# Optimization experiments

Measured on AMD Instinct MI355X. Metric: run time of the kernel, lower is better.

Reference implementation:

```python
import jax, jax.numpy as jnp
import numpy as np
import math

B, S, E, H = 4, 1024, 768, 12
HD = E // H

def setup_inputs() -> dict:
    key = jax.random.key(0)
    ks = jax.random.split(key, 13)
    inp = {
        'query': jax.random.normal(ks[0], (B, S, E), jnp.float32),
        'key':   jax.random.normal(ks[1], (B, S, E), jnp.float32),
        'value': jax.random.normal(ks[2], (B, S, E), jnp.float32),
        'mask':  jax.random.randint(ks[3], (B, S, S), 0, 2, jnp.int32),
    }
    scale = 1.0 / math.sqrt(E)
    for i, nm in enumerate(['q', 'k', 'v', 'o']):
        inp[f'W{nm}'] = jax.random.normal(ks[4 + 2 * i], (E, E), jnp.float32) * scale
        inp[f'b{nm}'] = jax.random.normal(ks[5 + 2 * i], (E,), jnp.float32) * 0.01
    return inp


def reference(query, key, value, mask, Wq, bq, Wk, bk, Wv, bv, Wo, bo):
    # QKV projections (torch Linear: x @ W.T + b), split into heads -> [B,H,S,HD]
    def proj(x, W, b):
        y = x @ W.T + b
        return y.reshape(B, S, H, HD).transpose(0, 2, 1, 3)

    q = proj(query, Wq, bq)
    k = proj(key, Wk, bk)
    v = proj(value, Wv, bv)

    scores = jnp.einsum('bhqd,bhkd->bhqk', q, k) / jnp.sqrt(jnp.float32(HD))
    m = mask[:, None, :, :]  # [B,1,S,S] broadcast over heads
    # multiply-then-masked_fill semantics of the original module
    scores = scores * m.astype(scores.dtype)
    scores = jnp.where(m == 0, -jnp.inf, scores)
    attn = jax.nn.softmax(scores, axis=-1)
    # nan_to_num for fully-masked rows (all -inf -> NaN -> 0)
    attn = jnp.where(jnp.isnan(attn), 0.0, attn)
    # dropout omitted (eval/deterministic reference)
    xv = jnp.einsum('bhqk,bhkd->bhqd', attn, v)
    xv = xv.transpose(0, 2, 1, 3).reshape(B, S, E)
    out = xv @ Wo.T + bo
    return out
```

## Files before the change

kernel.cpp:

```cpp
#include <hip/hip_runtime.h>

typedef __bf16 bf16x8 __attribute__((ext_vector_type(8)));
typedef float floatx4 __attribute__((ext_vector_type(4)));

#define B_ 4
#define S_ 1024
#define E_ 768
#define H_ 12
#define HD_ 64

__device__ __forceinline__ void async16(const void* g, void* l) {
  __builtin_amdgcn_global_load_lds((const __attribute__((address_space(1))) void*)g,
                                   (__attribute__((address_space(3))) void*)l, 16, 0, 0);
}

__device__ __forceinline__ floatx4 mfma16(bf16x8 a, bf16x8 b, floatx4 c) {
  return __builtin_amdgcn_mfma_f32_16x16x32_bf16(a, b, c, 0, 0, 0);
}

__device__ __forceinline__ bf16x8 cvt8(float4 a, float4 b) {
  bf16x8 o;
  o[0] = (__bf16)a.x; o[1] = (__bf16)a.y; o[2] = (__bf16)a.z; o[3] = (__bf16)a.w;
  o[4] = (__bf16)b.x; o[5] = (__bf16)b.y; o[6] = (__bf16)b.z; o[7] = (__bf16)b.w;
  return o;
}

__global__ __launch_bounds__(256) void prep_kernel(
    const float* __restrict__ w0, const float* __restrict__ w1,
    const float* __restrict__ w2, const float* __restrict__ w3,
    const int* __restrict__ mask,
    __bf16* __restrict__ wb, unsigned long long* __restrict__ bm) {
  const int bx = blockIdx.x;
  if (bx < 1152) {
    const int z = bx / 288, xb = bx % 288;
    const float* s = (z == 0) ? w0 : (z == 1) ? w1 : (z == 2) ? w2 : w3;
    __bf16* d = wb + (size_t)z * (size_t)(E_ * E_);
    const size_t i8 = (size_t)xb * 256 + threadIdx.x;
    const float4* sp = (const float4*)s + i8 * 2;
    *(bf16x8*)(d + i8 * 8) = cvt8(sp[0], sp[1]);
  } else {
    const int row0 = (bx - 1152) * 4;
    const int wave = threadIdx.x >> 6, lane = threadIdx.x & 63;
#pragma unroll
    for (int rr = 0; rr < 4; ++rr) {
      const int row = row0 + rr;
#pragma unroll
      for (int pass = 0; pass < 4; ++pass) {
        const int kk = pass * 256 + wave * 64 + lane;
        const int mv = mask[(size_t)row * S_ + kk];
        const unsigned long long bal = __ballot(mv != 0);
        if (lane == 0) bm[(size_t)row * 16 + pass * 4 + wave] = bal;
      }
    }
  }
}

__global__ __launch_bounds__(256, 3) void proj_qkv_kernel(
    const float* __restrict__ Xq, const float* __restrict__ Xk, const float* __restrict__ Xv,
    const __bf16* __restrict__ Wq, const __bf16* __restrict__ Wk, const __bf16* __restrict__ Wv,
    const float* __restrict__ bq, const float* __restrict__ bk, const float* __restrict__ bv,
    __bf16* __restrict__ Qf, __bf16* __restrict__ Kf, __bf16* __restrict__ Vt) {
  const int z = blockIdx.z;
  const float* X = (z == 0) ? Xq : (z == 1) ? Xk : Xv;
  const __bf16* W = (z == 0) ? Wq : (z == 1) ? Wk : Wv;
  const float* bias = (z == 0) ? bq : (z == 1) ? bk : bv;

  const int tid = threadIdx.x;
  const int wave = tid >> 6, lane = tid & 63;
  const int l15 = lane & 15, quad = lane >> 4;
  const int wr = wave >> 1, wc = wave & 1;
  const int bm = blockIdx.x * 128, bn = blockIdx.y * 128;
  const int srl = lane >> 3, sch = lane & 7;

  __shared__ alignas(16) unsigned char smem[36864];
  __bf16* ST = (__bf16*)smem + (size_t)wave * (64 * 72);

  floatx4 zf = {0.0f, 0.0f, 0.0f, 0.0f};
  floatx4 acc[4][4];
#pragma unroll
  for (int i = 0; i < 4; ++i)
#pragma unroll
    for (int j = 0; j < 4; ++j) acc[i][j] = zf;

#pragma unroll
  for (int c = 0; c < 4; ++c) {
    const int s = c * 4 + wave;
    const int row = s * 8 + srl;
    const int xo = (sch ^ (row & 7)) * 8;
    async16(W + (size_t)(bn + row) * E_ + xo, (__bf16*)smem + s * 512);
  }

  for (int kt = 0; kt < 12; ++kt) {
    const int p = kt & 1;
    __bf16* Bs = (__bf16*)(smem + p * 16384);
    __syncthreads();

    if (kt < 11) {
      const int kk = (kt + 1) * 64;
      __bf16* Bn = (__bf16*)(smem + (1 - p) * 16384);
#pragma unroll
      for (int c = 0; c < 4; ++c) {
        const int s = c * 4 + wave;
        const int row = s * 8 + srl;
        const int xo = (sch ^ (row & 7)) * 8;
        async16(W + (size_t)(bn + row) * E_ + kk + xo, Bn + s * 512);
      }
    }

    bf16x8 af[4][2];
#pragma unroll
    for (int i = 0; i < 4; ++i) {
      const float* xr = X + (size_t)(bm + wr * 64 + i * 16 + l15) * E_ + kt * 64 + quad * 8;
      float4 p0 = *(const float4*)(xr);
      float4 p1 = *(const float4*)(xr + 4);
      float4 p2 = *(const float4*)(xr + 32);
      float4 p3 = *(const float4*)(xr + 36);
      af[i][0] = cvt8(p0, p1);
      af[i][1] = cvt8(p2, p3);
    }

#pragma unroll
    for (int ks = 0; ks < 2; ++ks) {
      bf16x8 bfr[4];
#pragma unroll
      for (int j = 0; j < 4; ++j) {
        const int n = wc * 64 + j * 16 + l15;
        bfr[j] = *(const bf16x8*)&Bs[n * 64 + (((ks * 4 + quad) ^ (n & 7)) * 8)];
      }
#pragma unroll
      for (int i = 0; i < 4; ++i)
#pragma unroll
        for (int j = 0; j < 4; ++j)
          acc[i][j] = mfma16(af[i][ks], bfr[j], acc[i][j]);
    }
  }
  __syncthreads();

  if (z < 2) {
    __bf16* dst = (z == 0) ? Qf : Kf;
    const float sc = (z == 0) ? 0.125f : 1.0f;
#pragma unroll
    for (int j = 0; j < 4; ++j) {
      const float bval = bias[bn + wc * 64 + j * 16 + l15];
#pragma unroll
      for (int i = 0; i < 4; ++i)
#pragma unroll
        for (int r = 0; r < 4; ++r)
          ST[(i * 16 + quad * 4 + r) * 72 + j * 16 + l15] =
              (__bf16)((acc[i][j][r] + bval) * sc);
    }
#pragma unroll
    for (int t = 0; t < 8; ++t) {
      const int row = t * 8 + (lane >> 3), ch = lane & 7;
      bf16x8 vrow = *(const bf16x8*)&ST[row * 72 + ch * 8];
      *(bf16x8*)&dst[(size_t)(bm + wr * 64 + row) * E_ + bn + wc * 64 + ch * 8] = vrow;
    }
  } else {
#pragma unroll
    for (int j = 0; j < 4; ++j) {
      const float bval = bias[bn + wc * 64 + j * 16 + l15];
#pragma unroll
      for (int i = 0; i < 4; ++i)
#pragma unroll
        for (int r = 0; r < 4; ++r)
          ST[(j * 16 + l15) * 72 + i * 16 + quad * 4 + r] = (__bf16)(acc[i][j][r] + bval);
    }
    const int hh = (bn + wc * 64) >> 6;
    const int m0 = bm + wr * 64;
    const int bb = m0 >> 10, ss0 = m0 & 1023;
#pragma unroll
    for (int t = 0; t < 8; ++t) {
      const int d = t * 8 + (lane >> 3), ch = lane & 7;
      bf16x8 vrow = *(const bf16x8*)&ST[d * 72 + ch * 8];
      *(bf16x8*)&Vt[(((size_t)bb * H_ + hh) * HD_ + d) * S_ + ss0 + ch * 8] = vrow;
    }
  }
}

__global__ __launch_bounds__(256, 4) void proj_out_kernel(
    const __bf16* __restrict__ X, const __bf16* __restrict__ W,
    const float* __restrict__ bias, float* __restrict__ out) {
  const int tid = threadIdx.x;
  const int wave = tid >> 6, lane = tid & 63;
  const int l15 = lane & 15, quad = lane >> 4;
  const int wr = wave >> 1, wc = wave & 1;
  const int bm = blockIdx.x * 64, bn = blockIdx.y * 64;
  const int srl = lane >> 3, sch = lane & 7;

  __shared__ alignas(16) unsigned char smem[32768];

  floatx4 zf = {0.0f, 0.0f, 0.0f, 0.0f};
  floatx4 acc[2][2];
#pragma unroll
  for (int i = 0; i < 2; ++i)
#pragma unroll
    for (int j = 0; j < 2; ++j) acc[i][j] = zf;

#pragma unroll
  for (int c = 0; c < 2; ++c) {
    const int s = c * 4 + wave;
    const int row = s * 8 + srl;
    const int xo = (sch ^ (row & 7)) * 8;
    async16(X + (size_t)(bm + row) * E_ + xo, (__bf16*)smem + s * 512);
    async16(W + (size_t)(bn + row) * E_ + xo, (__bf16*)(smem + 8192) + s * 512);
  }

  for (int kt = 0; kt < 12; ++kt) {
    const int p = kt & 1;
    __bf16* As = (__bf16*)(smem + p * 16384);
    __bf16* Bs = (__bf16*)(smem + p * 16384 + 8192);
    __syncthreads();

    if (kt < 11) {
      const int kk = (kt + 1) * 64;
      __bf16* An = (__bf16*)(smem + (1 - p) * 16384);
      __bf16* Bn = (__bf16*)(smem + (1 - p) * 16384 + 8192);
#pragma unroll
      for (int c = 0; c < 2; ++c) {
        const int s = c * 4 + wave;
        const int row = s * 8 + srl;
        const int xo = (sch ^ (row & 7)) * 8;
        async16(X + (size_t)(bm + row) * E_ + kk + xo, An + s * 512);
        async16(W + (size_t)(bn + row) * E_ + kk + xo, Bn + s * 512);
      }
    }

#pragma unroll
    for (int ks = 0; ks < 2; ++ks) {
      bf16x8 af[2], bfr[2];
#pragma unroll
      for (int i = 0; i < 2; ++i) {
        const int m = wr * 32 + i * 16 + l15;
        af[i] = *(const bf16x8*)&As[m * 64 + (((ks * 4 + quad) ^ (m & 7)) * 8)];
      }
#pragma unroll
      for (int j = 0; j < 2; ++j) {
        const int n = wc * 32 + j * 16 + l15;
        bfr[j] = *(const bf16x8*)&Bs[n * 64 + (((ks * 4 + quad) ^ (n & 7)) * 8)];
      }
#pragma unroll
      for (int i = 0; i < 2; ++i)
#pragma unroll
        for (int j = 0; j < 2; ++j)
          acc[i][j] = mfma16(af[i], bfr[j], acc[i][j]);
    }
  }

#pragma unroll
  for (int j = 0; j < 2; ++j) {
    const int n = bn + wc * 32 + j * 16 + l15;
    const float bval = bias[n];
#pragma unroll
    for (int i = 0; i < 2; ++i) {
#pragma unroll
      for (int r = 0; r < 4; ++r) {
        const int m = bm + wr * 32 + i * 16 + quad * 4 + r;
        out[(size_t)m * E_ + n] = acc[i][j][r] + bval;
      }
    }
  }
}

#define MSHIFT 12.0f
#define PSTR 72
__global__ __launch_bounds__(256, 3) void attn_kernel(
    const __bf16* __restrict__ Qf, const __bf16* __restrict__ Kf,
    const __bf16* __restrict__ Vt, const unsigned long long* __restrict__ bmask,
    __bf16* __restrict__ XV) {
  const int tid = threadIdx.x;
  const int wave = tid >> 6, lane = tid & 63;
  const int l15 = lane & 15, quad = lane >> 4;
  const int bh = blockIdx.x;
  const int b = bh / H_, h = bh % H_;
  const int q0 = blockIdx.y * 64 + wave * 16;

  __shared__ alignas(16) __bf16 Kbuf[2][64 * 64];
  __shared__ alignas(16) __bf16 Vbuf[2][64 * 64];
  __shared__ alignas(16) __bf16 Ps[4 * 16 * PSTR];
  __bf16* Pw = &Ps[wave * 16 * PSTR];

  const __bf16* qb = Qf + ((size_t)b * S_ + q0) * E_ + h * HD_;
  bf16x8 af[2];
  af[0] = *(const bf16x8*)(qb + (size_t)l15 * E_ + quad * 8);
  af[1] = *(const bf16x8*)(qb + (size_t)l15 * E_ + 32 + quad * 8);

  const __bf16* kbase = Kf + (size_t)b * S_ * E_ + h * HD_;
  const __bf16* vbase = Vt + (size_t)bh * HD_ * S_;
  const unsigned long long* mbm = bmask + ((size_t)b * S_ + q0) * 16;

  const int srow = tid >> 3, sch = tid & 7;
#pragma unroll
  for (int c = 0; c < 2; ++c) {
    const int row = c * 32 + srow;
    const int xo = (sch ^ (row & 7)) * 8;
    async16(kbase + (size_t)row * E_ + xo, &Kbuf[0][(c * 256 + tid) * 8]);
    async16(vbase + (size_t)row * S_ + xo, &Vbuf[0][(c * 256 + tid) * 8]);
  }

  unsigned long long bmsh[4];
#pragma unroll
  for (int r = 0; r < 4; ++r)
    bmsh[r] = mbm[(size_t)(quad * 4 + r) * 16 + 0] >> l15;

  floatx4 zf = {0.0f, 0.0f, 0.0f, 0.0f};
  floatx4 o[4];
  float lrow[4];
#pragma unroll
  for (int jd = 0; jd < 4; ++jd) o[jd] = zf;
#pragma unroll
  for (int r = 0; r < 4; ++r) lrow[r] = 0.0f;

  for (int kt = 0; kt < 16; ++kt) {
    const int p = kt & 1;
    const int k0 = kt * 64;
    __syncthreads();

    if (kt < 15) {
      const int kn = k0 + 64;
#pragma unroll
      for (int c = 0; c < 2; ++c) {
        const int row = c * 32 + srow;
        const int xo = (sch ^ (row & 7)) * 8;
        async16(kbase + (size_t)(kn + row) * E_ + xo, &Kbuf[1 - p][(c * 256 + tid) * 8]);
        async16(vbase + (size_t)row * S_ + kn + xo, &Vbuf[1 - p][(c * 256 + tid) * 8]);
      }
    }

    unsigned long long bmnext[4];
    if (kt < 15) {
#pragma unroll
      for (int r = 0; r < 4; ++r)
        bmnext[r] = mbm[(size_t)(quad * 4 + r) * 16 + kt + 1] >> l15;
    }

    bf16x8 bk[4][2];
#pragma unroll
    for (int j = 0; j < 4; ++j) {
      const int key = j * 16 + l15;
#pragma unroll
      for (int ks = 0; ks < 2; ++ks)
        bk[j][ks] = *(const bf16x8*)&Kbuf[p][key * 64 + ((ks * 4 + quad) ^ (key & 7)) * 8];
    }
    bf16x8 bvf[4][2];
#pragma unroll
    for (int jd = 0; jd < 4; ++jd) {
      const int d = jd * 16 + l15;
#pragma unroll
      for (int ks2 = 0; ks2 < 2; ++ks2)
        bvf[jd][ks2] = *(const bf16x8*)&Vbuf[p][d * 64 + ((ks2 * 4 + quad) ^ (d & 7)) * 8];
    }

    floatx4 sc[4];
#pragma unroll
    for (int j = 0; j < 4; ++j) sc[j] = zf;
#pragma unroll
    for (int j = 0; j < 4; ++j) {
      sc[j] = mfma16(af[0], bk[j][0], sc[j]);
      sc[j] = mfma16(af[1], bk[j][1], sc[j]);
    }

#pragma unroll
    for (int j = 0; j < 4; ++j)
#pragma unroll
      for (int r = 0; r < 4; ++r) {
        float pv = __expf(sc[j][r] - MSHIFT);
        pv = ((bmsh[r] >> (j * 16)) & 1ull) ? pv : 0.0f;
        lrow[r] += pv;
        Pw[(quad * 4 + r) * PSTR + j * 16 + l15] = (__bf16)pv;
      }

#pragma unroll
    for (int ks2 = 0; ks2 < 2; ++ks2) {
      bf16x8 pa = *(const bf16x8*)&Pw[l15 * PSTR + ks2 * 32 + quad * 8];
#pragma unroll
      for (int jd = 0; jd < 4; ++jd) o[jd] = mfma16(pa, bvf[jd][ks2], o[jd]);
    }

    if (kt < 15) {
#pragma unroll
      for (int r = 0; r < 4; ++r) bmsh[r] = bmnext[r];
    }
  }

#pragma unroll
  for (int sh = 1; sh < 16; sh <<= 1)
#pragma unroll
    for (int r = 0; r < 4; ++r) lrow[r] += __shfl_xor(lrow[r], sh, 64);
  float linv[4];
#pragma unroll
  for (int r = 0; r < 4; ++r) linv[r] = (lrow[r] > 0.0f) ? (1.0f / lrow[r]) : 0.0f;
  __bf16* xbase = XV + ((size_t)b * S_ + q0) * E_ + h * HD_;
#pragma unroll
  for (int jd = 0; jd < 4; ++jd)
#pragma unroll
    for (int r = 0; r < 4; ++r)
      xbase[(size_t)(quad * 4 + r) * E_ + jd * 16 + l15] = (__bf16)(o[jd][r] * linv[r]);
}

extern "C" void kernel_launch(void* const* d_in, const int* in_sizes, int n_in,
                              void* d_out, int out_size, void* d_ws, size_t ws_size,
                              hipStream_t stream) {
  const float* query = (const float*)d_in[0];
  const float* key   = (const float*)d_in[1];
  const float* value = (const float*)d_in[2];
  const int*   mask  = (const int*)d_in[3];
  const float* Wq = (const float*)d_in[4];
  const float* bq = (const float*)d_in[5];
  const float* Wk = (const float*)d_in[6];
  const float* bk = (const float*)d_in[7];
  const float* Wv = (const float*)d_in[8];
  const float* bv = (const float*)d_in[9];
  const float* Wo = (const float*)d_in[10];
  const float* bo = (const float*)d_in[11];
  float* out = (float*)d_out;

  const size_t NX = (size_t)B_ * S_ * E_;
  const size_t NW = (size_t)E_ * E_;
  __bf16* ws = (__bf16*)d_ws;
  __bf16* wqb = ws;
  __bf16* wkb = wqb + NW;
  __bf16* wvb = wkb + NW;
  __bf16* wob = wvb + NW;
  __bf16* Qf  = wob + NW;
  __bf16* Kf  = Qf + NX;
  __bf16* Vt  = Kf + NX;
  __bf16* XVb = Vt + NX;
  unsigned long long* bmask = (unsigned long long*)(XVb + NX);

  prep_kernel<<<dim3(2176), 256, 0, stream>>>(Wq, Wk, Wv, Wo, mask, wqb, bmask);
  proj_qkv_kernel<<<dim3(32, 6, 3), 256, 0, stream>>>(query, key, value,
                                                      wqb, wkb, wvb, bq, bk, bv,
                                                      Qf, Kf, Vt);
  attn_kernel<<<dim3(48, 16), 256, 0, stream>>>(Qf, Kf, Vt, bmask, XVb);
  proj_out_kernel<<<dim3(64, 12), 256, 0, stream>>>(XVb, wob, bo, out);
}
```

Baseline: 224.1 us.

## Stage fp32 activations through LDS with async double-buffered loads in QKV projection

The QKV projection kernel now loads the fp32 X tile into LDS with asynchronous global-to-LDS copies, double-buffered alongside the weight tile. Previously each wave read X directly from global memory with no prefetch. The K step is halved to 32 so the fp32 tile fits, giving 24 iterations instead of 12, with a new swizzled layout for both operands. The change aims to hide global latency for the activation operand, at the cost of more LDS (48KB, which may lower occupancy under the launch bounds) and twice as many barriers.

```diff
diff --git a/kernel.cpp b/kernel.cpp
--- a/kernel.cpp
+++ b/kernel.cpp
@@ -72,7 +72,7 @@
   const int bm = blockIdx.x * 128, bn = blockIdx.y * 128;
   const int srl = lane >> 3, sch = lane & 7;
 
-  __shared__ alignas(16) unsigned char smem[36864];
+  __shared__ alignas(16) unsigned char smem[49152];
   __bf16* ST = (__bf16*)smem + (size_t)wave * (64 * 72);
 
   floatx4 zf = {0.0f, 0.0f, 0.0f, 0.0f};
@@ -82,59 +82,67 @@
 #pragma unroll
     for (int j = 0; j < 4; ++j) acc[i][j] = zf;
 
-#pragma unroll
-  for (int c = 0; c < 4; ++c) {
-    const int s = c * 4 + wave;
-    const int row = s * 8 + srl;
-    const int xo = (sch ^ (row & 7)) * 8;
-    async16(W + (size_t)(bn + row) * E_ + xo, (__bf16*)smem + s * 512);
-  }
-
-  for (int kt = 0; kt < 12; ++kt) {
+#define STAGE_A(buf, kt)                                                        \
+  {                                                                             \
+    _Pragma("unroll") for (int c = 0; c < 4; ++c) {                             \
+      const int s = c * 4 + wave;                                               \
+      const int row = s * 8 + srl;                                              \
+      const int xo = (sch ^ (row & 7)) * 4;                                     \
+      async16(X + (size_t)(bm + row) * E_ + (kt) * 32 + xo,                     \
+              (char*)(buf) + (s * 64 + lane) * 16);                             \
+    }                                                                           \
+  }
+#define STAGE_B(buf, kt)                                                        \
+  {                                                                             \
+    _Pragma("unroll") for (int c = 0; c < 2; ++c) {                             \
+      const int s = wave * 2 + c;                                               \
+      const int l = s * 8 + srl;                                                \
+      const int u = sch ^ (l & 7);                                              \
+      const int row = l + ((u >> 2) << 6);                                      \
+      const int ch = u & 3;                                                     \
+      async16(W + (size_t)(bn + row) * E_ + (kt) * 32 + ch * 8,                 \
+              (char*)(buf) + (s * 64 + lane) * 16);                             \
+    }                                                                           \
+  }
+
+  STAGE_A(smem, 0);
+  STAGE_B(smem + 32768, 0);
+
+  for (int kt = 0; kt < 24; ++kt) {
     const int p = kt & 1;
-    __bf16* Bs = (__bf16*)(smem + p * 16384);
+    const float* As = (const float*)(smem + p * 16384);
+    const __bf16* Bs = (const __bf16*)(smem + 32768 + p * 8192);
     __syncthreads();
 
-    if (kt < 11) {
-      const int kk = (kt + 1) * 64;
-      __bf16* Bn = (__bf16*)(smem + (1 - p) * 16384);
-#pragma unroll
-      for (int c = 0; c < 4; ++c) {
-        const int s = c * 4 + wave;
-        const int row = s * 8 + srl;
-        const int xo = (sch ^ (row & 7)) * 8;
-        async16(W + (size_t)(bn + row) * E_ + kk + xo, Bn + s * 512);
-      }
-    }
-
-    bf16x8 af[4][2];
+    if (kt < 23) {
+      STAGE_A(smem + (1 - p) * 16384, kt + 1);
+      STAGE_B(smem + 32768 + (1 - p) * 8192, kt + 1);
+    }
+
+    bf16x8 af[4];
 #pragma unroll
     for (int i = 0; i < 4; ++i) {
-      const float* xr = X + (size_t)(bm + wr * 64 + i * 16 + l15) * E_ + kt * 64 + quad * 8;
-      float4 p0 = *(const float4*)(xr);
-      float4 p1 = *(const float4*)(xr + 4);
-      float4 p2 = *(const float4*)(xr + 32);
-      float4 p3 = *(const float4*)(xr + 36);
-      af[i][0] = cvt8(p0, p1);
-      af[i][1] = cvt8(p2, p3);
-    }
-
-#pragma unroll
-    for (int ks = 0; ks < 2; ++ks) {
-      bf16x8 bfr[4];
-#pragma unroll
-      for (int j = 0; j < 4; ++j) {
-        const int n = wc * 64 + j * 16 + l15;
-        bfr[j] = *(const bf16x8*)&Bs[n * 64 + (((ks * 4 + quad) ^ (n & 7)) * 8)];
-      }
-#pragma unroll
-      for (int i = 0; i < 4; ++i)
-#pragma unroll
-        for (int j = 0; j < 4; ++j)
-          acc[i][j] = mfma16(af[i][ks], bfr[j], acc[i][j]);
-    }
+      const int m = wr * 64 + i * 16 + l15;
+      float4 f0 = *(const float4*)((const char*)As + m * 128 + (((2 * quad) ^ (m & 7)) * 16));
+      float4 f1 = *(const float4*)((const char*)As + m * 128 + (((2 * quad + 1) ^ (m & 7)) * 16));
+      af[i] = cvt8(f0, f1);
+    }
+    bf16x8 bfr[4];
+#pragma unroll
+    for (int j = 0; j < 4; ++j) {
+      const int nl = j * 16 + l15;
+      bfr[j] = *(const bf16x8*)((const char*)Bs + nl * 128 +
+                                (((wc * 4 + quad) ^ (nl & 7)) * 16));
+    }
+#pragma unroll
+    for (int i = 0; i < 4; ++i)
+#pragma unroll
+      for (int j = 0; j < 4; ++j)
+        acc[i][j] = mfma16(af[i], bfr[j], acc[i][j]);
   }
   __syncthreads();
+#undef STAGE_A
+#undef STAGE_B
 
   if (z < 2) {
     __bf16* dst = (z == 0) ? Qf : Kf;
```

Measured after the change: 188.4 us. 15.9% less time.
